# Kernel tuning notes

Hardware: AMD Instinct MI355X
Metric: run time of the kernel (lower is better)

## Reference

```python
import jax, jax.numpy as jnp
import numpy as np

N, F = 16384, 32
H1, H2, D1, D2 = 64, 64, 32, 1


def setup_inputs() -> dict:
    key = jax.random.key(0)
    ks = jax.random.split(key, 10)
    x = jax.random.normal(ks[0], (N, F), dtype=jnp.float32)
    # pre-normalized adjacency (GCNConv expects D^-1/2 A D^-1/2); mimic with uniform/N
    a = jax.random.uniform(ks[1], (N, N), dtype=jnp.float32) / N
    # glorot-ish scaled params
    W1 = jax.random.normal(ks[2], (F, H1), dtype=jnp.float32) * (1.0 / np.sqrt(F))
    b1 = jnp.zeros((H1,), dtype=jnp.float32)
    W2 = jax.random.normal(ks[3], (H1, H2), dtype=jnp.float32) * (1.0 / np.sqrt(H1))
    b2 = jnp.zeros((H2,), dtype=jnp.float32)
    Wd1 = jax.random.normal(ks[4], (H2, D1), dtype=jnp.float32) * (1.0 / np.sqrt(H2))
    bd1 = jnp.zeros((D1,), dtype=jnp.float32)
    Wd2 = jax.random.normal(ks[5], (D1, D2), dtype=jnp.float32) * (1.0 / np.sqrt(D1))
    bd2 = jnp.zeros((D2,), dtype=jnp.float32)
    return {"x": x, "a": a, "W1": W1, "b1": b1, "W2": W2, "b2": b2,
            "Wd1": Wd1, "bd1": bd1, "Wd2": Wd2, "bd2": bd2}


def reference(x, a, W1, b1, W2, b2, Wd1, bd1, Wd2, bd2):
    # GCNConv: relu(a @ (x @ W) + b)   (a is pre-normalized)
    g1 = jax.nn.relu(a @ (x @ W1) + b1)   # [N, 64]
    g2 = jax.nn.relu(a @ (g1 @ W2) + b2)  # [N, 64]
    d3 = jax.nn.relu(g2 @ Wd1 + bd1)      # [N, 32]
    return d3 @ Wd2 + bd2                 # [N, 1]
```

## Files before the change

kernel.cpp:

```cpp
#include <hip/hip_runtime.h>
#include <hip/hip_bf16.h>


typedef __bf16 bf16x8 __attribute__((ext_vector_type(8)));
typedef float  f32x16 __attribute__((ext_vector_type(16)));
typedef float  f32x4v __attribute__((ext_vector_type(4)));
typedef int    i32x4  __attribute__((ext_vector_type(4)));

#define NNODE 16384
#define KDIM  16384
#define HCOL  64

__device__ inline i32x4 pack8(f32x4v a, f32x4v b){
  bf16x8 t;
  t[0]=(__bf16)a[0]; t[1]=(__bf16)a[1]; t[2]=(__bf16)a[2]; t[3]=(__bf16)a[3];
  t[4]=(__bf16)b[0]; t[5]=(__bf16)b[1]; t[6]=(__bf16)b[2]; t[7]=(__bf16)b[3];
  return __builtin_bit_cast(i32x4, t);
}
#define BC(x) __builtin_bit_cast(bf16x8, x)

__global__ __launch_bounds__(256, 1) void gcn_layer_kernel(
    const float* __restrict__ A,
    const __bf16* __restrict__ Ht,
    const float* __restrict__ bias,
    float* __restrict__ G)
{
  __shared__ i32x4 sA[4*2*512];
  __shared__ i32x4 sH[4*2*512];

  const int tid  = threadIdx.x;
  const int lane = tid & 63;
  const int kw   = tid >> 6;
  const int row0 = blockIdx.x * 64;

  const int rA0  = lane >> 3;
  const int ccA  = lane & 7;
  const int swzA = ccA ^ rA0;
  const int r    = lane & 31;
  const int hsub = lane >> 5;
  const int xs   = r & 7;

  const size_t k0 = (size_t)kw * 4096;

  f32x4v ra[16]; i32x4 rh[8];

  const float* pA0 = A + (size_t)(row0 + rA0) * KDIM + k0 + (size_t)ccA*8;
  const i32x4* pH0 = (const i32x4*)Ht + (size_t)rA0 * (KDIM/8) + k0/8 + ccA;

  auto stage_load = [&](int t){
    const float* pA = pA0 + (size_t)t*64;
    #pragma unroll
    for (int pi=0; pi<8; ++pi){
      const float* p = pA + (size_t)pi*8*KDIM;
      ra[2*pi]   = __builtin_nontemporal_load((const f32x4v*)p);
      ra[2*pi+1] = __builtin_nontemporal_load((const f32x4v*)(p+4));
    }
    const i32x4* pH = pH0 + (size_t)t*8;
    #pragma unroll
    for (int pi=0; pi<8; ++pi)
      rh[pi] = pH[(size_t)pi*8*(KDIM/8)];
  };

  auto stage_write = [&](int buf){
    i32x4* dA = &sA[(kw*2+buf)*512];
    #pragma unroll
    for (int pi=0; pi<8; ++pi)
      dA[(rA0 + pi*8)*8 + swzA] = pack8(ra[2*pi], ra[2*pi+1]);
    i32x4* dH = &sH[(kw*2+buf)*512];
    #pragma unroll
    for (int pi=0; pi<8; ++pi)
      dH[(rA0 + pi*8)*8 + swzA] = rh[pi];
  };

  f32x16 acc00 = {}, acc01 = {}, acc10 = {}, acc11 = {};

  auto compute = [&](int buf){
    const i32x4* bA = &sA[(kw*2+buf)*512];
    const i32x4* bH = &sH[(kw*2+buf)*512];
    #pragma unroll
    for (int kk=0; kk<4; ++kk){
      int c = (kk*2 + hsub) ^ xs;
      bf16x8 a0 = BC(bA[r*8 + c]);
      bf16x8 a1 = BC(bA[(r+32)*8 + c]);
      bf16x8 b0 = BC(bH[r*8 + c]);
      bf16x8 b1 = BC(bH[(r+32)*8 + c]);
      acc00 = __builtin_amdgcn_mfma_f32_32x32x16_bf16(a0, b0, acc00, 0,0,0);
      acc01 = __builtin_amdgcn_mfma_f32_32x32x16_bf16(a0, b1, acc01, 0,0,0);
      acc10 = __builtin_amdgcn_mfma_f32_32x32x16_bf16(a1, b0, acc10, 0,0,0);
      acc11 = __builtin_amdgcn_mfma_f32_32x32x16_bf16(a1, b1, acc11, 0,0,0);
    }
  };

  stage_load(0);
  stage_write(0);
  stage_load(1);
  #pragma unroll 1
  for (int t=0; t<63; ++t){
    compute(t&1);
    stage_write((t+1)&1);
    if (t < 62) stage_load(t+2);
  }
  compute(1);

  __syncthreads();

  float* red = (float*)sA;
  if (kw > 0){
    float* rd = red + (size_t)(kw-1)*4096;
    #pragma unroll
    for (int j=0; j<16; ++j){
      int rr = (j&3) + 8*(j>>2) + 4*hsub;
      rd[(rr   )*64 + r]      = acc00[j];
      rd[(rr   )*64 + 32 + r] = acc01[j];
      rd[(rr+32)*64 + r]      = acc10[j];
      rd[(rr+32)*64 + 32 + r] = acc11[j];
    }
  }
  __syncthreads();
  if (kw == 0){
    #pragma unroll
    for (int j=0; j<16; ++j){
      int rr = (j&3) + 8*(j>>2) + 4*hsub;
      float v00 = acc00[j] + red[(rr   )*64+r]    + red[4096+(rr   )*64+r]    + red[8192+(rr   )*64+r]    + bias[r];
      float v01 = acc01[j] + red[(rr   )*64+32+r] + red[4096+(rr   )*64+32+r] + red[8192+(rr   )*64+32+r] + bias[32+r];
      float v10 = acc10[j] + red[(rr+32)*64+r]    + red[4096+(rr+32)*64+r]    + red[8192+(rr+32)*64+r]    + bias[r];
      float v11 = acc11[j] + red[(rr+32)*64+32+r] + red[4096+(rr+32)*64+32+r] + red[8192+(rr+32)*64+32+r] + bias[32+r];
      G[(size_t)(row0 + rr     )*HCOL + r]      = fmaxf(v00, 0.f);
      G[(size_t)(row0 + rr     )*HCOL + 32 + r] = fmaxf(v01, 0.f);
      G[(size_t)(row0 + rr + 32)*HCOL + r]      = fmaxf(v10, 0.f);
      G[(size_t)(row0 + rr + 32)*HCOL + 32 + r] = fmaxf(v11, 0.f);
    }
  }
}

template<int F>
__global__ __launch_bounds__(128) void proj_T_kernel(
    const float* __restrict__ in,
    const float* __restrict__ W,
    __bf16* __restrict__ out)
{
  constexpr int FP = F + 4;
  __shared__ float sWt[64*FP];
  __shared__ short sOut[64*136];

  int tid = threadIdx.x;
  for (int e = tid; e < 64*F; e += 128){
    int h = e / F, j = e - h*F;
    sWt[h*FP + j] = W[j*64 + h];
  }
  __syncthreads();

  const size_t n = (size_t)blockIdx.x*128 + tid;
  float rowv[F];
  #pragma unroll
  for (int j=0; j<F; j+=4){
    f32x4v v = *(const f32x4v*)(in + n*F + j);
    rowv[j]=v[0]; rowv[j+1]=v[1]; rowv[j+2]=v[2]; rowv[j+3]=v[3];
  }
  #pragma unroll
  for (int h=0; h<64; ++h){
    float s = 0.f;
    #pragma unroll
    for (int j=0; j<F; j+=4){
      f32x4v w = *(const f32x4v*)&sWt[h*FP + j];
      s += rowv[j]*w[0] + rowv[j+1]*w[1] + rowv[j+2]*w[2] + rowv[j+3]*w[3];
    }
    sOut[h*136 + tid] = __builtin_bit_cast(short, (__bf16)s);
  }
  __syncthreads();

  const size_t n0 = (size_t)blockIdx.x*128;
  #pragma unroll
  for (int pi=0; pi<8; ++pi){
    int p = pi*128 + tid;
    int h = p >> 4, cc = p & 15;
    i32x4 v = *(const i32x4*)&sOut[h*136 + cc*8];
    *(i32x4*)(out + (size_t)h*NNODE + n0 + cc*8) = v;
  }
}

__global__ __launch_bounds__(256) void tail_kernel(
    const float* __restrict__ g2,
    const float* __restrict__ Wd1,
    const float* __restrict__ bd1,
    const float* __restrict__ Wd2,
    const float* __restrict__ bd2,
    float* __restrict__ outp)
{
  __shared__ float sW[64*32];
  __shared__ float sb1[32], sw2[32];
  int tid = threadIdx.x;
  for (int e=tid; e<2048; e+=256) sW[e] = Wd1[e];
  if (tid < 32){ sb1[tid] = bd1[tid]; sw2[tid] = Wd2[tid]; }
  __syncthreads();

  size_t n = (size_t)blockIdx.x*256 + tid;
  float rv[64];
  #pragma unroll
  for (int j=0;j<64;j+=4){
    f32x4v v = *(const f32x4v*)(g2 + n*64 + j);
    rv[j]=v[0]; rv[j+1]=v[1]; rv[j+2]=v[2]; rv[j+3]=v[3];
  }
  float o = 0.f;
  #pragma unroll
  for (int c=0;c<32;++c){
    float s = sb1[c];
    #pragma unroll
    for (int j=0;j<64;++j) s += rv[j]*sW[j*32 + c];
    o += fmaxf(s, 0.f) * sw2[c];
  }
  outp[n] = o + bd2[0];
}

extern "C" void kernel_launch(void* const* d_in, const int* in_sizes, int n_in,
                              void* d_out, int out_size, void* d_ws, size_t ws_size,
                              hipStream_t stream)
{
  const float* x   = (const float*)d_in[0];
  const float* a   = (const float*)d_in[1];
  const float* W1  = (const float*)d_in[2];
  const float* b1  = (const float*)d_in[3];
  const float* W2  = (const float*)d_in[4];
  const float* b2  = (const float*)d_in[5];
  const float* Wd1 = (const float*)d_in[6];
  const float* bd1 = (const float*)d_in[7];
  const float* Wd2 = (const float*)d_in[8];
  const float* bd2 = (const float*)d_in[9];
  float* outp = (float*)d_out;

  char* ws = (char*)d_ws;
  __bf16* Ht1 = (__bf16*)(ws);
  __bf16* Ht2 = (__bf16*)(ws + (2u<<20));
  float*  g1  = (float*)(ws + (4u<<20));
  float*  g2  = (float*)(ws + (8u<<20));

  proj_T_kernel<32><<<128, 128, 0, stream>>>(x,  W1, Ht1);
  gcn_layer_kernel <<<256, 256, 0, stream>>>(a, Ht1, b1, g1);
  proj_T_kernel<64><<<128, 128, 0, stream>>>(g1, W2, Ht2);
  gcn_layer_kernel <<<256, 256, 0, stream>>>(a, Ht2, b2, g2);
  tail_kernel      <<<64, 256, 0, stream>>>(g2, Wd1, bd1, Wd2, bd2, outp);
}
```

Measured before the change: 453.8 us.

## Split GCN aggregation K dimension across two blocks with 512-thread workgroups

```diff
diff --git a/kernel.cpp b/kernel.cpp
--- a/kernel.cpp
+++ b/kernel.cpp
@@ -19,71 +19,77 @@
 }
 #define BC(x) __builtin_bit_cast(bf16x8, x)
 
-__global__ __launch_bounds__(256, 1) void gcn_layer_kernel(
+__global__ __launch_bounds__(512, 2) void gcn_layer_kernel(
     const float* __restrict__ A,
     const __bf16* __restrict__ Ht,
-    const float* __restrict__ bias,
-    float* __restrict__ G)
-{
-  __shared__ i32x4 sA[4*2*512];
-  __shared__ i32x4 sH[4*2*512];
+    float* __restrict__ gP)
+{
+  __shared__ i32x4 smem[8192];
 
   const int tid  = threadIdx.x;
   const int lane = tid & 63;
-  const int kw   = tid >> 6;
-  const int row0 = blockIdx.x * 64;
-
-  const int rA0  = lane >> 3;
-  const int ccA  = lane & 7;
-  const int swzA = ccA ^ rA0;
+  const int wid  = tid >> 6;
+  const int kw   = wid & 3;
+  const int rh   = wid >> 2;
+  const int bid  = blockIdx.x;
+  const int kh   = bid & 1;
+  const int rowblk = bid >> 1;
+  const int rowbase = rowblk*128 + rh*64;
+
+  const int srow = lane >> 2;
+  const int cc   = lane & 3;
+  const int swz  = cc ^ (srow & 3);
   const int r    = lane & 31;
   const int hsub = lane >> 5;
-  const int xs   = r & 7;
-
-  const size_t k0 = (size_t)kw * 4096;
-
-  f32x4v ra[16]; i32x4 rh[8];
-
-  const float* pA0 = A + (size_t)(row0 + rA0) * KDIM + k0 + (size_t)ccA*8;
-  const i32x4* pH0 = (const i32x4*)Ht + (size_t)rA0 * (KDIM/8) + k0/8 + ccA;
+  const int x3   = r & 3;
+
+  const size_t k0 = (size_t)kh*8192 + (size_t)kw*2048;
+
+  i32x4* sAw = smem + wid*512;
+  i32x4* sHw = smem + 4096 + wid*512;
+
+  f32x4v ra[8]; i32x4 rhh[4];
+
+  const float*  pA0 = A  + (size_t)(rowbase + srow)*KDIM + k0 + (size_t)cc*8;
+  const __bf16* pH0 = Ht + (size_t)srow*KDIM           + k0 + (size_t)cc*8;
 
   auto stage_load = [&](int t){
-    const float* pA = pA0 + (size_t)t*64;
-    #pragma unroll
-    for (int pi=0; pi<8; ++pi){
-      const float* p = pA + (size_t)pi*8*KDIM;
+    const float* pA = pA0 + (size_t)t*32;
+    #pragma unroll
+    for (int pi=0; pi<4; ++pi){
+      const float* p = pA + (size_t)pi*16*KDIM;
       ra[2*pi]   = __builtin_nontemporal_load((const f32x4v*)p);
       ra[2*pi+1] = __builtin_nontemporal_load((const f32x4v*)(p+4));
     }
-    const i32x4* pH = pH0 + (size_t)t*8;
-    #pragma unroll
-    for (int pi=0; pi<8; ++pi)
-      rh[pi] = pH[(size_t)pi*8*(KDIM/8)];
+    const __bf16* pH = pH0 + (size_t)t*32;
+    #pragma unroll
+    for (int pi=0; pi<4; ++pi)
+      rhh[pi] = *(const i32x4*)(pH + (size_t)pi*16*KDIM);
   };
 
   auto stage_write = [&](int buf){
-    i32x4* dA = &sA[(kw*2+buf)*512];
-    #pragma unroll
-    for (int pi=0; pi<8; ++pi)
-      dA[(rA0 + pi*8)*8 + swzA] = pack8(ra[2*pi], ra[2*pi+1]);
-    i32x4* dH = &sH[(kw*2+buf)*512];
-    #pragma unroll
-    for (int pi=0; pi<8; ++pi)
-      dH[(rA0 + pi*8)*8 + swzA] = rh[pi];
+    i32x4* dA = sAw + buf*256;
+    #pragma unroll
+    for (int pi=0; pi<4; ++pi)
+      dA[(pi*16 + srow)*4 + swz] = pack8(ra[2*pi], ra[2*pi+1]);
+    i32x4* dH = sHw + buf*256;
+    #pragma unroll
+    for (int pi=0; pi<4; ++pi)
+      dH[(pi*16 + srow)*4 + swz] = rhh[pi];
   };
 
   f32x16 acc00 = {}, acc01 = {}, acc10 = {}, acc11 = {};
 
   auto compute = [&](int buf){
-    const i32x4* bA = &sA[(kw*2+buf)*512];
-    const i32x4* bH = &sH[(kw*2+buf)*512];
-    #pragma unroll
-    for (int kk=0; kk<4; ++kk){
-      int c = (kk*2 + hsub) ^ xs;
-      bf16x8 a0 = BC(bA[r*8 + c]);
-      bf16x8 a1 = BC(bA[(r+32)*8 + c]);
-      bf16x8 b0 = BC(bH[r*8 + c]);
-      bf16x8 b1 = BC(bH[(r+32)*8 + c]);
+    const i32x4* bA = sAw + buf*256;
+    const i32x4* bH = sHw + buf*256;
+    #pragma unroll
+    for (int kk=0; kk<2; ++kk){
+      int c = (kk*2 + hsub) ^ x3;
+      bf16x8 a0 = BC(bA[r*4 + c]);
+      bf16x8 a1 = BC(bA[(r+32)*4 + c]);
+      bf16x8 b0 = BC(bH[r*4 + c]);
+      bf16x8 b1 = BC(bH[(r+32)*4 + c]);
       acc00 = __builtin_amdgcn_mfma_f32_32x32x16_bf16(a0, b0, acc00, 0,0,0);
       acc01 = __builtin_amdgcn_mfma_f32_32x32x16_bf16(a0, b1, acc01, 0,0,0);
       acc10 = __builtin_amdgcn_mfma_f32_32x32x16_bf16(a1, b0, acc10, 0,0,0);
@@ -104,9 +110,9 @@
 
   __syncthreads();
 
-  float* red = (float*)sA;
+  float* red = (float*)smem;
   if (kw > 0){
-    float* rd = red + (size_t)(kw-1)*4096;
+    float* rd = red + rh*12288 + (size_t)(kw-1)*4096;
     #pragma unroll
     for (int j=0; j<16; ++j){
       int rr = (j&3) + 8*(j>>2) + 4*hsub;
@@ -118,19 +124,38 @@
   }
   __syncthreads();
   if (kw == 0){
+    float* rd = red + rh*12288;
+    float* out = gP + ((size_t)kh*NNODE + rowbase)*HCOL;
     #pragma unroll
     for (int j=0; j<16; ++j){
       int rr = (j&3) + 8*(j>>2) + 4*hsub;
-      float v00 = acc00[j] + red[(rr   )*64+r]    + red[4096+(rr   )*64+r]    + red[8192+(rr   )*64+r]    + bias[r];
-      float v01 = acc01[j] + red[(rr   )*64+32+r] + red[4096+(rr   )*64+32+r] + red[8192+(rr   )*64+32+r] + bias[32+r];
-      float v10 = acc10[j] + red[(rr+32)*64+r]    + red[4096+(rr+32)*64+r]    + red[8192+(rr+32)*64+r]    + bias[r];
-      float v11 = acc11[j] + red[(rr+32)*64+32+r] + red[4096+(rr+32)*64+32+r] + red[8192+(rr+32)*64+32+r] + bias[32+r];
-      G[(size_t)(row0 + rr     )*HCOL + r]      = fmaxf(v00, 0.f);
-      G[(size_t)(row0 + rr     )*HCOL + 32 + r] = fmaxf(v01, 0.f);
-      G[(size_t)(row0 + rr + 32)*HCOL + r]      = fmaxf(v10, 0.f);
-      G[(size_t)(row0 + rr + 32)*HCOL + 32 + r] = fmaxf(v11, 0.f);
-    }
-  }
+      float v00 = acc00[j] + rd[(rr   )*64+r]    + rd[4096+(rr   )*64+r]    + rd[8192+(rr   )*64+r];
+      float v01 = acc01[j] + rd[(rr   )*64+32+r] + rd[4096+(rr   )*64+32+r] + rd[8192+(rr   )*64+32+r];
+      float v10 = acc10[j] + rd[(rr+32)*64+r]    + rd[4096+(rr+32)*64+r]    + rd[8192+(rr+32)*64+r];
+      float v11 = acc11[j] + rd[(rr+32)*64+32+r] + rd[4096+(rr+32)*64+32+r] + rd[8192+(rr+32)*64+32+r];
+      out[(size_t)(rr     )*HCOL + r]      = v00;
+      out[(size_t)(rr     )*HCOL + 32 + r] = v01;
+      out[(size_t)(rr + 32)*HCOL + r]      = v10;
+      out[(size_t)(rr + 32)*HCOL + 32 + r] = v11;
+    }
+  }
+}
+
+__global__ __launch_bounds__(256) void reduce_kernel(
+    const float* __restrict__ gP,
+    const float* __restrict__ bias,
+    float* __restrict__ g)
+{
+  const size_t i = (size_t)blockIdx.x * 256 + threadIdx.x;
+  const f32x4v* p = (const f32x4v*)gP;
+  f32x4v s = p[i] + p[i + 262144];
+  f32x4v b = *(const f32x4v*)(bias + (i & 15) * 4);
+  f32x4v o;
+  o[0] = fmaxf(s[0] + b[0], 0.f);
+  o[1] = fmaxf(s[1] + b[1], 0.f);
+  o[2] = fmaxf(s[2] + b[2], 0.f);
+  o[3] = fmaxf(s[3] + b[3], 0.f);
+  ((f32x4v*)g)[i] = o;
 }
 
 template<int F>
@@ -233,10 +258,13 @@
   __bf16* Ht2 = (__bf16*)(ws + (2u<<20));
   float*  g1  = (float*)(ws + (4u<<20));
   float*  g2  = (float*)(ws + (8u<<20));
+  float*  gP  = (float*)(ws + (12u<<20));
 
   proj_T_kernel<32><<<128, 128, 0, stream>>>(x,  W1, Ht1);
-  gcn_layer_kernel <<<256, 256, 0, stream>>>(a, Ht1, b1, g1);
+  gcn_layer_kernel <<<256, 512, 0, stream>>>(a, Ht1, gP);
+  reduce_kernel    <<<1024, 256, 0, stream>>>(gP, b1, g1);
   proj_T_kernel<64><<<128, 128, 0, stream>>>(g1, W2, Ht2);
-  gcn_layer_kernel <<<256, 256, 0, stream>>>(a, Ht2, b2, g2);
+  gcn_layer_kernel <<<256, 512, 0, stream>>>(a, Ht2, gP);
+  reduce_kernel    <<<1024, 256, 0, stream>>>(gP, b2, g2);
   tail_kernel      <<<64, 256, 0, stream>>>(g2, Wd1, bd1, Wd2, bd2, outp);
 }
```

Result: slower. 519.2 us (+14.4%).

## Share H tile across waves and split K across blocks with separate reduction

Applied to the files above, without the earlier changes.

```diff
diff --git a/kernel.cpp b/kernel.cpp
--- a/kernel.cpp
+++ b/kernel.cpp
@@ -22,16 +22,17 @@
 __global__ __launch_bounds__(256, 1) void gcn_layer_kernel(
     const float* __restrict__ A,
     const __bf16* __restrict__ Ht,
-    const float* __restrict__ bias,
-    float* __restrict__ G)
+    float* __restrict__ gP)
 {
   __shared__ i32x4 sA[4*2*512];
-  __shared__ i32x4 sH[4*2*512];
+  __shared__ i32x4 sH[2*512];
 
   const int tid  = threadIdx.x;
   const int lane = tid & 63;
-  const int kw   = tid >> 6;
-  const int row0 = blockIdx.x * 64;
+  const int wid  = tid >> 6;
+  const int bid  = blockIdx.x;
+  const int kq   = bid & 3;
+  const int row0 = (bid >> 2) * 256 + wid * 64;
 
   const int rA0  = lane >> 3;
   const int ccA  = lane & 7;
@@ -40,12 +41,15 @@
   const int hsub = lane >> 5;
   const int xs   = r & 7;
 
-  const size_t k0 = (size_t)kw * 4096;
-
-  f32x4v ra[16]; i32x4 rh[8];
+  const int hrow = tid >> 2;
+  const int cc2  = (tid & 3) * 2;
+
+  const size_t k0 = (size_t)kq * 4096;
+
+  f32x4v ra[16]; i32x4 rh[2];
 
   const float* pA0 = A + (size_t)(row0 + rA0) * KDIM + k0 + (size_t)ccA*8;
-  const i32x4* pH0 = (const i32x4*)Ht + (size_t)rA0 * (KDIM/8) + k0/8 + ccA;
+  const i32x4* pH0 = (const i32x4*)(Ht + (size_t)hrow * KDIM + k0) + cc2;
 
   auto stage_load = [&](int t){
     const float* pA = pA0 + (size_t)t*64;
@@ -55,28 +59,25 @@
       ra[2*pi]   = __builtin_nontemporal_load((const f32x4v*)p);
       ra[2*pi+1] = __builtin_nontemporal_load((const f32x4v*)(p+4));
     }
-    const i32x4* pH = pH0 + (size_t)t*8;
-    #pragma unroll
-    for (int pi=0; pi<8; ++pi)
-      rh[pi] = pH[(size_t)pi*8*(KDIM/8)];
+    rh[0] = pH0[(size_t)t*8];
+    rh[1] = pH0[(size_t)t*8 + 1];
   };
 
   auto stage_write = [&](int buf){
-    i32x4* dA = &sA[(kw*2+buf)*512];
+    i32x4* dA = &sA[(wid*2+buf)*512];
     #pragma unroll
     for (int pi=0; pi<8; ++pi)
       dA[(rA0 + pi*8)*8 + swzA] = pack8(ra[2*pi], ra[2*pi+1]);
-    i32x4* dH = &sH[(kw*2+buf)*512];
-    #pragma unroll
-    for (int pi=0; pi<8; ++pi)
-      dH[(rA0 + pi*8)*8 + swzA] = rh[pi];
+    i32x4* dH = &sH[buf*512 + hrow*8];
+    dH[cc2 ^ (hrow & 7)]       = rh[0];
+    dH[(cc2+1) ^ (hrow & 7)]   = rh[1];
   };
 
   f32x16 acc00 = {}, acc01 = {}, acc10 = {}, acc11 = {};
 
   auto compute = [&](int buf){
-    const i32x4* bA = &sA[(kw*2+buf)*512];
-    const i32x4* bH = &sH[(kw*2+buf)*512];
+    const i32x4* bA = &sA[(wid*2+buf)*512];
+    const i32x4* bH = &sH[buf*512];
     #pragma unroll
     for (int kk=0; kk<4; ++kk){
       int c = (kk*2 + hsub) ^ xs;
@@ -94,43 +95,47 @@
   stage_load(0);
   stage_write(0);
   stage_load(1);
+  __syncthreads();
   #pragma unroll 1
   for (int t=0; t<63; ++t){
+    int nx = t+2; if (nx > 63) nx = 63;
     compute(t&1);
+    __syncthreads();
     stage_write((t+1)&1);
-    if (t < 62) stage_load(t+2);
+    stage_load(nx);
+    __syncthreads();
   }
   compute(1);
 
-  __syncthreads();
-
-  float* red = (float*)sA;
-  if (kw > 0){
-    float* rd = red + (size_t)(kw-1)*4096;
-    #pragma unroll
-    for (int j=0; j<16; ++j){
-      int rr = (j&3) + 8*(j>>2) + 4*hsub;
-      rd[(rr   )*64 + r]      = acc00[j];
-      rd[(rr   )*64 + 32 + r] = acc01[j];
-      rd[(rr+32)*64 + r]      = acc10[j];
-      rd[(rr+32)*64 + 32 + r] = acc11[j];
-    }
-  }
-  __syncthreads();
-  if (kw == 0){
-    #pragma unroll
-    for (int j=0; j<16; ++j){
-      int rr = (j&3) + 8*(j>>2) + 4*hsub;
-      float v00 = acc00[j] + red[(rr   )*64+r]    + red[4096+(rr   )*64+r]    + red[8192+(rr   )*64+r]    + bias[r];
-      float v01 = acc01[j] + red[(rr   )*64+32+r] + red[4096+(rr   )*64+32+r] + red[8192+(rr   )*64+32+r] + bias[32+r];
-      float v10 = acc10[j] + red[(rr+32)*64+r]    + red[4096+(rr+32)*64+r]    + red[8192+(rr+32)*64+r]    + bias[r];
-      float v11 = acc11[j] + red[(rr+32)*64+32+r] + red[4096+(rr+32)*64+32+r] + red[8192+(rr+32)*64+32+r] + bias[32+r];
-      G[(size_t)(row0 + rr     )*HCOL + r]      = fmaxf(v00, 0.f);
-      G[(size_t)(row0 + rr     )*HCOL + 32 + r] = fmaxf(v01, 0.f);
-      G[(size_t)(row0 + rr + 32)*HCOL + r]      = fmaxf(v10, 0.f);
-      G[(size_t)(row0 + rr + 32)*HCOL + 32 + r] = fmaxf(v11, 0.f);
-    }
-  }
+  float* out = gP + ((size_t)kq * NNODE + row0) * HCOL;
+  #pragma unroll
+  for (int j=0; j<16; ++j){
+    int rr = (j&3) + 8*(j>>2) + 4*hsub;
+    out[(size_t)(rr     )*HCOL + r]      = acc00[j];
+    out[(size_t)(rr     )*HCOL + 32 + r] = acc01[j];
+    out[(size_t)(rr + 32)*HCOL + r]      = acc10[j];
+    out[(size_t)(rr + 32)*HCOL + 32 + r] = acc11[j];
+  }
+}
+
+__global__ __launch_bounds__(256) void reduce_kernel(
+    const float* __restrict__ gP,
+    const float* __restrict__ bias,
+    float* __restrict__ g)
+{
+  const size_t i = (size_t)blockIdx.x * 256 + threadIdx.x;
+  const f32x4v* p = (const f32x4v*)gP;
+  f32x4v s = p[i];
+  s += p[i +  262144];
+  s += p[i +  524288];
+  s += p[i +  786432];
+  f32x4v b = *(const f32x4v*)(bias + (i & 15) * 4);
+  f32x4v o;
+  o[0] = fmaxf(s[0] + b[0], 0.f);
+  o[1] = fmaxf(s[1] + b[1], 0.f);
+  o[2] = fmaxf(s[2] + b[2], 0.f);
+  o[3] = fmaxf(s[3] + b[3], 0.f);
+  ((f32x4v*)g)[i] = o;
 }
 
 template<int F>
@@ -233,10 +238,13 @@
   __bf16* Ht2 = (__bf16*)(ws + (2u<<20));
   float*  g1  = (float*)(ws + (4u<<20));
   float*  g2  = (float*)(ws + (8u<<20));
+  float*  gP  = (float*)(ws + (12u<<20));
 
   proj_T_kernel<32><<<128, 128, 0, stream>>>(x,  W1, Ht1);
-  gcn_layer_kernel <<<256, 256, 0, stream>>>(a, Ht1, b1, g1);
+  gcn_layer_kernel <<<256, 256, 0, stream>>>(a, Ht1, gP);
+  reduce_kernel    <<<1024, 256, 0, stream>>>(gP, b1, g1);
   proj_T_kernel<64><<<128, 128, 0, stream>>>(g1, W2, Ht2);
-  gcn_layer_kernel <<<256, 256, 0, stream>>>(a, Ht2, b2, g2);
+  gcn_layer_kernel <<<256, 256, 0, stream>>>(a, Ht2, gP);
+  reduce_kernel    <<<1024, 256, 0, stream>>>(gP, b2, g2);
   tail_kernel      <<<64, 256, 0, stream>>>(g2, Wd1, bd1, Wd2, bd2, outp);
 }
```

After: 495.9 us. 1.09x slower.

## Load H operand directly from global and double the per-stage K tile

Applied to the files above, without the earlier changes.

```diff
diff --git a/kernel.cpp b/kernel.cpp
--- a/kernel.cpp
+++ b/kernel.cpp
@@ -25,8 +25,7 @@
     const float* __restrict__ bias,
     float* __restrict__ G)
 {
-  __shared__ i32x4 sA[4*2*512];
-  __shared__ i32x4 sH[4*2*512];
+  __shared__ i32x4 sA[4*2*1024];
 
   const int tid  = threadIdx.x;
   const int lane = tid & 63;
@@ -35,55 +34,58 @@
 
   const int rA0  = lane >> 3;
   const int ccA  = lane & 7;
-  const int swzA = ccA ^ rA0;
+  const int swz8 = ccA ^ rA0;
   const int r    = lane & 31;
   const int hsub = lane >> 5;
   const int xs   = r & 7;
 
   const size_t k0 = (size_t)kw * 4096;
 
-  f32x4v ra[16]; i32x4 rh[8];
+  f32x4v ra[32];
 
   const float* pA0 = A + (size_t)(row0 + rA0) * KDIM + k0 + (size_t)ccA*8;
-  const i32x4* pH0 = (const i32x4*)Ht + (size_t)rA0 * (KDIM/8) + k0/8 + ccA;
+  const __bf16* pB0 = Ht + (size_t)r * KDIM + k0 + (size_t)hsub*8;
+  const __bf16* pB1 = pB0 + (size_t)32 * KDIM;
 
   auto stage_load = [&](int t){
-    const float* pA = pA0 + (size_t)t*64;
-    #pragma unroll
-    for (int pi=0; pi<8; ++pi){
-      const float* p = pA + (size_t)pi*8*KDIM;
-      ra[2*pi]   = __builtin_nontemporal_load((const f32x4v*)p);
-      ra[2*pi+1] = __builtin_nontemporal_load((const f32x4v*)(p+4));
-    }
-    const i32x4* pH = pH0 + (size_t)t*8;
-    #pragma unroll
-    for (int pi=0; pi<8; ++pi)
-      rh[pi] = pH[(size_t)pi*8*(KDIM/8)];
+    const float* pA = pA0 + (size_t)t*128;
+    #pragma unroll
+    for (int gg=0; gg<8; ++gg){
+      const float* p = pA + (size_t)gg*8*KDIM;
+      #pragma unroll
+      for (int s=0; s<2; ++s){
+        ra[gg*4+s*2+0] = __builtin_nontemporal_load((const f32x4v*)(p + s*64));
+        ra[gg*4+s*2+1] = __builtin_nontemporal_load((const f32x4v*)(p + s*64 + 4));
+      }
+    }
   };
 
   auto stage_write = [&](int buf){
-    i32x4* dA = &sA[(kw*2+buf)*512];
-    #pragma unroll
-    for (int pi=0; pi<8; ++pi)
-      dA[(rA0 + pi*8)*8 + swzA] = pack8(ra[2*pi], ra[2*pi+1]);
-    i32x4* dH = &sH[(kw*2+buf)*512];
-    #pragma unroll
-    for (int pi=0; pi<8; ++pi)
-      dH[(rA0 + pi*8)*8 + swzA] = rh[pi];
+    i32x4* dA = &sA[(kw*2+buf)*1024];
+    #pragma unroll
+    for (int gg=0; gg<8; ++gg){
+      #pragma unroll
+      for (int s=0; s<2; ++s){
+        int cp = (s<<3) | swz8;
+        dA[(rA0 + gg*8)*16 + cp] = pack8(ra[gg*4+s*2+0], ra[gg*4+s*2+1]);
+      }
+    }
   };
 
   f32x16 acc00 = {}, acc01 = {}, acc10 = {}, acc11 = {};
 
-  auto compute = [&](int buf){
-    const i32x4* bA = &sA[(kw*2+buf)*512];
-    const i32x4* bH = &sH[(kw*2+buf)*512];
-    #pragma unroll
-    for (int kk=0; kk<4; ++kk){
-      int c = (kk*2 + hsub) ^ xs;
-      bf16x8 a0 = BC(bA[r*8 + c]);
-      bf16x8 a1 = BC(bA[(r+32)*8 + c]);
-      bf16x8 b0 = BC(bH[r*8 + c]);
-      bf16x8 b1 = BC(bH[(r+32)*8 + c]);
+  auto compute = [&](int buf, int t){
+    const i32x4* bA = &sA[(kw*2+buf)*1024];
+    const __bf16* q0 = pB0 + (size_t)t*128;
+    const __bf16* q1 = pB1 + (size_t)t*128;
+    #pragma unroll
+    for (int kk=0; kk<8; ++kk){
+      int c  = kk*2 + hsub;
+      int cp = (c & 8) | ((c & 7) ^ xs);
+      bf16x8 a0 = BC(bA[r*16 + cp]);
+      bf16x8 a1 = BC(bA[(r+32)*16 + cp]);
+      bf16x8 b0 = BC(*(const i32x4*)(q0 + kk*16));
+      bf16x8 b1 = BC(*(const i32x4*)(q1 + kk*16));
       acc00 = __builtin_amdgcn_mfma_f32_32x32x16_bf16(a0, b0, acc00, 0,0,0);
       acc01 = __builtin_amdgcn_mfma_f32_32x32x16_bf16(a0, b1, acc01, 0,0,0);
       acc10 = __builtin_amdgcn_mfma_f32_32x32x16_bf16(a1, b0, acc10, 0,0,0);
@@ -95,12 +97,12 @@
   stage_write(0);
   stage_load(1);
   #pragma unroll 1
-  for (int t=0; t<63; ++t){
-    compute(t&1);
+  for (int t=0; t<31; ++t){
+    compute(t&1, t);
     stage_write((t+1)&1);
-    if (t < 62) stage_load(t+2);
-  }
-  compute(1);
+    if (t < 30) stage_load(t+2);
+  }
+  compute(1, 31);
 
   __syncthreads();
 
```

Measured after the change: 554.6 us. 22.2% more time.
